# Optimization experiments

Hardware: AMD Instinct MI355X
Metric: run time of the kernel (lower is better)

Reference implementation:

```python
import jax, jax.numpy as jnp
from jax import lax
import numpy as np

EPS = 1e-5  # BatchNorm eps


def setup_inputs() -> dict:
    key = jax.random.key(0)
    ks = jax.random.split(key, 4)
    T, B, C = 256, 128, 1024
    L, H, NCLS = 6, 1024, 1000
    x = jax.random.normal(ks[0], (T, B, C), dtype=jnp.float32)
    W = jax.random.normal(ks[1], (L, C, H), dtype=jnp.float32) * (1.0 / np.sqrt(C))
    b = jnp.zeros((L, H), dtype=jnp.float32)
    gamma = jnp.ones((L, H), dtype=jnp.float32)
    beta = jnp.zeros((L, H), dtype=jnp.float32)
    u = jax.random.uniform(ks[2], (L, H), dtype=jnp.float32)  # recurrent weights in (0, U_bound~1)
    Wc = jax.random.normal(ks[3], (H, NCLS), dtype=jnp.float32) * (1.0 / np.sqrt(H))
    bc = jnp.zeros((NCLS,), dtype=jnp.float32)
    return {"x": x, "W": W, "b": b, "gamma": gamma, "beta": beta, "u": u, "Wc": Wc, "bc": bc}


def _layer(h, Wl, bl, gl, betal, ul):
    # per-timestep dense projection: [T,B,Cin] @ [Cin,H]
    z = jnp.einsum('tbi,ih->tbh', h, Wl) + bl
    # BN over (time, batch) per channel (bn_before, training-mode batch stats)
    mean = jnp.mean(z, axis=(0, 1))
    var = jnp.var(z, axis=(0, 1))
    z = (z - mean) * (gl / jnp.sqrt(var + EPS)) + betal
    # IndRNN diagonal recurrence: h_t = relu(z_t + u * h_{t-1}), h_0 = 0
    T, B, H = z.shape
    def step(hprev, zt):
        hnew = jax.nn.relu(zt + ul * hprev)
        return hnew, hnew
    _, hs = lax.scan(step, jnp.zeros((B, H), dtype=z.dtype), z)
    return hs


def reference(x, W, b, gamma, beta, u, Wc, bc):
    h = x
    for l in range(W.shape[0]):
        h = _layer(h, W[l], b[l], gamma[l], beta[l], u[l])
    # classifier on last timestep
    return h[-1] @ Wc + bc
```

## Files before the change

kernel.cpp:

```cpp
#include <hip/hip_runtime.h>
#include <hip/hip_bf16.h>

#define T_DIM 256
#define B_DIM 128
#define C_DIM 1024
#define H_DIM 1024
#define L_DIM 6
#define NC_DIM 1000
#define M_DIM (T_DIM * B_DIM)
#define BH_DIM (B_DIM * H_DIM)

typedef __attribute__((ext_vector_type(8))) short bf16x8;
typedef __attribute__((ext_vector_type(4))) float f32x4;

__device__ __forceinline__ float bf2f(unsigned short u) {
  union { unsigned int i; float f; } v; v.i = ((unsigned int)u) << 16; return v.f;
}
__device__ __forceinline__ unsigned short f2bf(float f) {
  union { float f; unsigned int i; } v; v.f = f;
  unsigned int r = v.i + 0x7fffu + ((v.i >> 16) & 1u);
  return (unsigned short)(r >> 16);
}

__device__ __forceinline__ void gload_lds16(const void* g, void* l) {
  __builtin_amdgcn_global_load_lds(
      (const __attribute__((address_space(1))) unsigned int*)g,
      (__attribute__((address_space(3))) unsigned int*)l, 16, 0, 0);
}

__global__ __launch_bounds__(256) void f32_to_bf16_kernel(
    const float* __restrict__ in, unsigned short* __restrict__ out, int n4) {
  int stride = gridDim.x * blockDim.x;
  for (int i = blockIdx.x * blockDim.x + threadIdx.x; i < n4; i += stride) {
    float4 v = ((const float4*)in)[i];
    ushort4 o;
    o.x = f2bf(v.x); o.y = f2bf(v.y); o.z = f2bf(v.z); o.w = f2bf(v.w);
    ((ushort4*)out)[i] = o;
  }
}

__global__ __launch_bounds__(256) void wtrans_kernel(
    const float* __restrict__ W, unsigned short* __restrict__ Wt) {
  __shared__ float tile[32][33];
  int l = blockIdx.z;
  const float* Wl = W + (size_t)l * C_DIM * H_DIM;
  unsigned short* Wtl = Wt + (size_t)l * C_DIM * H_DIM;
  int h0 = blockIdx.x * 32, c0 = blockIdx.y * 32;
  int tx = threadIdx.x, ty = threadIdx.y;
#pragma unroll
  for (int i = 0; i < 32; i += 8)
    tile[ty + i][tx] = Wl[(size_t)(c0 + ty + i) * H_DIM + h0 + tx];
  __syncthreads();
#pragma unroll
  for (int i = 0; i < 32; i += 8)
    Wtl[(size_t)(h0 + ty + i) * C_DIM + c0 + tx] = f2bf(tile[tx][ty + i]);
}

#define NT 32

__global__ __launch_bounds__(512, 2) void gemm_kernel(
    const unsigned short* __restrict__ A, const unsigned short* __restrict__ Bt,
    unsigned short* __restrict__ Z, float* __restrict__ psum, float* __restrict__ psqs) {
  extern __shared__ char lds[];
  int bid = blockIdx.x;
  int swz = (bid & 7) * 64 + (bid >> 3);
  int tm = swz >> 2, tn = swz & 3;
  int tid = threadIdx.x;
  int wv = tid >> 6, ln = tid & 63;
  int wm = wv >> 2, wn = wv & 3;

  const char* Asrc = (const char*)A + (size_t)tm * 256 * 2048;
  const char* Bsrc = (const char*)Bt + (size_t)tn * 256 * 2048;
  int p0 = wv * 1024 + ln * 16;
  int p1 = 8192 + wv * 1024 + ln * 16;
  int l0 = p0 ^ (((p0 >> 7) & 3) << 4);
  int l1 = p1 ^ (((p1 >> 7) & 3) << 4);
  int ro0 = (p0 >> 6) * 2048 + (l0 & 63);
  int ro1 = (p1 >> 6) * 2048 + (l1 & 63);
  int dst0 = wv * 1024;
  int dst1 = 8192 + wv * 1024;

  int laneoff = (ln & 15) * 64 + ((((ln >> 4) ^ ((ln & 15) >> 1)) & 3) << 4);

  f32x4 acc[8][4];
  f32x4 zero = {0.f, 0.f, 0.f, 0.f};
#pragma unroll
  for (int m = 0; m < 8; ++m)
#pragma unroll
    for (int n = 0; n < 4; ++n) acc[m][n] = zero;

  auto stage = [&](int t) {
    char* ldsb = lds + ((t & 3) * 32768);
    int ko = t * 64;
    gload_lds16(Asrc + ro0 + ko, ldsb + dst0);
    gload_lds16(Asrc + ro1 + ko, ldsb + dst1);
    gload_lds16(Bsrc + ro0 + ko, ldsb + 16384 + dst0);
    gload_lds16(Bsrc + ro1 + ko, ldsb + 16384 + dst1);
  };

  auto body = [&](int t, bool dostage) {
    const char* buf = lds + ((t & 3) * 32768);
    const char* Ab = buf + wm * 8192;
    const char* Bb = buf + 16384 + wn * 4096;
    bf16x8 bf[4], a0[4], a1[4];
#pragma unroll
    for (int n = 0; n < 4; ++n) bf[n] = *(const bf16x8*)(Bb + n * 1024 + laneoff);
#pragma unroll
    for (int m = 0; m < 4; ++m) a0[m] = *(const bf16x8*)(Ab + m * 1024 + laneoff);
#pragma unroll
    for (int m = 0; m < 4; ++m) a1[m] = *(const bf16x8*)(Ab + 4096 + m * 1024 + laneoff);
    if (dostage) stage(t + 3);
    __builtin_amdgcn_s_setprio(1);
#pragma unroll
    for (int m = 0; m < 4; ++m)
#pragma unroll
      for (int n = 0; n < 4; ++n)
        acc[m][n] = __builtin_amdgcn_mfma_f32_16x16x32_bf16(a0[m], bf[n], acc[m][n], 0, 0, 0);
#pragma unroll
    for (int m = 0; m < 4; ++m)
#pragma unroll
      for (int n = 0; n < 4; ++n)
        acc[m + 4][n] = __builtin_amdgcn_mfma_f32_16x16x32_bf16(a1[m], bf[n], acc[m + 4][n], 0, 0, 0);
    __builtin_amdgcn_s_setprio(0);
  };

  stage(0); stage(1); stage(2);
  asm volatile("s_waitcnt vmcnt(8)" ::: "memory");
  __builtin_amdgcn_s_barrier();

  for (int t = 0; t < NT - 3; ++t) {
    body(t, true);
    asm volatile("s_waitcnt vmcnt(8)" ::: "memory");
    __builtin_amdgcn_s_barrier();
  }
  body(NT - 3, false);
  asm volatile("s_waitcnt vmcnt(4)" ::: "memory");
  __builtin_amdgcn_s_barrier();
  body(NT - 2, false);
  asm volatile("s_waitcnt vmcnt(0)" ::: "memory");
  __builtin_amdgcn_s_barrier();
  body(NT - 1, false);

  float s[4], q[4];
#pragma unroll
  for (int n = 0; n < 4; ++n) {
    float sv = 0.f, qv = 0.f;
#pragma unroll
    for (int m = 0; m < 8; ++m)
#pragma unroll
      for (int r = 0; r < 4; ++r) {
        float v = acc[m][n][r];
        sv += v; qv += v * v;
      }
    s[n] = sv; q[n] = qv;
  }
#pragma unroll
  for (int n = 0; n < 4; ++n) {
    s[n] += __shfl_xor(s[n], 16); s[n] += __shfl_xor(s[n], 32);
    q[n] += __shfl_xor(q[n], 16); q[n] += __shfl_xor(q[n], 32);
  }
  float* red = (float*)lds;
  if (ln < 16) {
#pragma unroll
    for (int n = 0; n < 4; ++n) {
      red[wm * 256 + wn * 64 + n * 16 + ln] = s[n];
      red[512 + wm * 256 + wn * 64 + n * 16 + ln] = q[n];
    }
  }
  __syncthreads();
  if (tid < 256) {
    psum[(size_t)tm * H_DIM + tn * 256 + tid] = red[tid] + red[256 + tid];
  } else {
    int c = tid - 256;
    psqs[(size_t)tm * H_DIM + tn * 256 + c] = red[512 + c] + red[768 + c];
  }
  int r0 = tm * 256 + wm * 128 + ((ln >> 4) << 2);
  int c0 = tn * 256 + wn * 64 + (ln & 15);
#pragma unroll
  for (int m = 0; m < 8; ++m)
#pragma unroll
    for (int n = 0; n < 4; ++n) {
      unsigned short* zp = Z + (size_t)(r0 + m * 16) * H_DIM + c0 + n * 16;
#pragma unroll
      for (int r = 0; r < 4; ++r) zp[(size_t)r * H_DIM] = f2bf(acc[m][n][r]);
    }
}

__global__ __launch_bounds__(256) void bn_finalize_kernel(
    const float* __restrict__ psum, const float* __restrict__ psqs,
    const float* __restrict__ gamma, const float* __restrict__ beta,
    float* __restrict__ ss) {
  int c = blockIdx.x * blockDim.x + threadIdx.x;
  float s = 0.f, q = 0.f;
  for (int i = 0; i < 128; ++i) {
    s += psum[(size_t)i * H_DIM + c];
    q += psqs[(size_t)i * H_DIM + c];
  }
  const float invN = 1.0f / (float)M_DIM;
  float mean = s * invN;
  float var = q * invN - mean * mean;
  float sc = gamma[c] * rsqrtf(var + 1e-5f);
  ss[c] = sc;
  ss[H_DIM + c] = beta[c] - mean * sc;
}

__global__ __launch_bounds__(256) void bn_recur_kernel(
    const unsigned short* __restrict__ Z, const float* __restrict__ ss,
    const float* __restrict__ u, unsigned short* __restrict__ Hout) {
  int i2 = blockIdx.x * 256 + threadIdx.x;
  int h0 = (i2 & (H_DIM / 2 - 1)) * 2;
  float sc0 = ss[h0], sc1 = ss[h0 + 1];
  float sh0 = ss[H_DIM + h0], sh1 = ss[H_DIM + h0 + 1];
  float u0 = u[h0], u1 = u[h0 + 1];
  float hv0 = 0.f, hv1 = 0.f;
  const unsigned int* Zp = (const unsigned int*)Z;
#pragma unroll 8
  for (int t = 0; t < T_DIM; ++t) {
    unsigned int zz = Zp[(size_t)t * (BH_DIM / 2) + i2];
    float z0 = fmaf(bf2f((unsigned short)(zz & 0xffffu)), sc0, sh0);
    float z1 = fmaf(bf2f((unsigned short)(zz >> 16)), sc1, sh1);
    hv0 = fmaxf(fmaf(u0, hv0, z0), 0.f);
    hv1 = fmaxf(fmaf(u1, hv1, z1), 0.f);
    ushort2 o; o.x = f2bf(hv0); o.y = f2bf(hv1);
    ((ushort2*)Hout)[(size_t)t * (BH_DIM / 2) + i2] = o;
  }
}

__global__ __launch_bounds__(256) void classifier_kernel(
    const unsigned short* __restrict__ hlast, const float* __restrict__ Wc,
    const float* __restrict__ bc, float* __restrict__ out) {
  __shared__ float hs[H_DIM];
  int b = blockIdx.y;
  int n = blockIdx.x * 256 + threadIdx.x;
  for (int k = threadIdx.x; k < H_DIM; k += 256)
    hs[k] = bf2f(hlast[(size_t)b * H_DIM + k]);
  __syncthreads();
  if (n < NC_DIM) {
    float acc = bc[n];
#pragma unroll 8
    for (int k = 0; k < H_DIM; ++k)
      acc = fmaf(hs[k], Wc[(size_t)k * NC_DIM + n], acc);
    out[(size_t)b * NC_DIM + n] = acc;
  }
}

extern "C" void kernel_launch(void* const* d_in, const int* in_sizes, int n_in,
                              void* d_out, int out_size, void* d_ws, size_t ws_size,
                              hipStream_t stream) {
  const float* x     = (const float*)d_in[0];
  const float* W     = (const float*)d_in[1];
  const float* gamma = (const float*)d_in[3];
  const float* beta  = (const float*)d_in[4];
  const float* u     = (const float*)d_in[5];
  const float* Wc    = (const float*)d_in[6];
  const float* bc    = (const float*)d_in[7];
  float* out = (float*)d_out;

  const size_t CH = (size_t)C_DIM * H_DIM;
  const size_t MH = (size_t)M_DIM * H_DIM;
  char* p = (char*)d_ws;
  unsigned short* Wt = (unsigned short*)p; p += L_DIM * CH * sizeof(unsigned short);
  unsigned short* Ha = (unsigned short*)p; p += MH * sizeof(unsigned short);
  unsigned short* Hb = (unsigned short*)p; p += MH * sizeof(unsigned short);
  unsigned short* Z  = (unsigned short*)p; p += MH * sizeof(unsigned short);
  float* psum = (float*)p; p += 128 * H_DIM * sizeof(float);
  float* psqs = (float*)p; p += 128 * H_DIM * sizeof(float);
  float* ss   = (float*)p; p += 2 * H_DIM * sizeof(float);

  f32_to_bf16_kernel<<<2048, 256, 0, stream>>>(x, Ha, (int)(MH / 4));
  wtrans_kernel<<<dim3(H_DIM / 32, C_DIM / 32, L_DIM), dim3(32, 8), 0, stream>>>(W, Wt);

  unsigned short* cur = Ha;
  unsigned short* nxt = Hb;
  for (int l = 0; l < L_DIM; ++l) {
    gemm_kernel<<<(M_DIM / 256) * (H_DIM / 256), 512, 131072, stream>>>(
        cur, Wt + (size_t)l * CH, Z, psum, psqs);
    bn_finalize_kernel<<<4, 256, 0, stream>>>(psum, psqs, gamma + (size_t)l * H_DIM,
                                              beta + (size_t)l * H_DIM, ss);
    bn_recur_kernel<<<BH_DIM / 512, 256, 0, stream>>>(Z, ss, u + (size_t)l * H_DIM, nxt);
    unsigned short* tmp = cur; cur = nxt; nxt = tmp;
  }
  classifier_kernel<<<dim3(4, B_DIM), 256, 0, stream>>>(
      cur + (size_t)(T_DIM - 1) * BH_DIM, Wc, bc, out);
}
```

Measured before the change: 782.0 us.

## Shrink GEMM tile to 256x128 with double-buffered LDS for higher occupancy

The GEMM tile shrinks from 256x256 to 256x128, with 8 waves arranged 4x2 and 16 accumulators each instead of 32. The LDS pipeline drops from 4-stage to 2-stage (48KB instead of 128KB), which allows more blocks per CU and doubles the grid. The BN partial-sum reduction is reworked to match the new wave layout, and the recurrence loop unroll goes from 8 to 16. The trade-off is less data reuse per block, more global traffic for the A operand, and a shallower prefetch, since each step now does a full vmcnt(0) wait.

```diff
diff --git a/kernel.cpp b/kernel.cpp
--- a/kernel.cpp
+++ b/kernel.cpp
@@ -58,87 +58,77 @@
 
 #define NT 32
 
-__global__ __launch_bounds__(512, 2) void gemm_kernel(
+__global__ __launch_bounds__(512, 4) void gemm_kernel(
     const unsigned short* __restrict__ A, const unsigned short* __restrict__ Bt,
     unsigned short* __restrict__ Z, float* __restrict__ psum, float* __restrict__ psqs) {
   extern __shared__ char lds[];
   int bid = blockIdx.x;
-  int swz = (bid & 7) * 64 + (bid >> 3);
-  int tm = swz >> 2, tn = swz & 3;
+  int swz = (bid & 7) * 128 + (bid >> 3);
+  int tm = swz >> 3, tn = swz & 7;
   int tid = threadIdx.x;
   int wv = tid >> 6, ln = tid & 63;
-  int wm = wv >> 2, wn = wv & 3;
+  int wm = wv >> 1, wn = wv & 1;
 
   const char* Asrc = (const char*)A + (size_t)tm * 256 * 2048;
-  const char* Bsrc = (const char*)Bt + (size_t)tn * 256 * 2048;
+  const char* Bsrc = (const char*)Bt + (size_t)tn * 128 * 2048;
   int p0 = wv * 1024 + ln * 16;
   int p1 = 8192 + wv * 1024 + ln * 16;
+  int pB = wv * 1024 + ln * 16;
   int l0 = p0 ^ (((p0 >> 7) & 3) << 4);
   int l1 = p1 ^ (((p1 >> 7) & 3) << 4);
+  int lB = pB ^ (((pB >> 7) & 3) << 4);
   int ro0 = (p0 >> 6) * 2048 + (l0 & 63);
   int ro1 = (p1 >> 6) * 2048 + (l1 & 63);
+  int roB = (pB >> 6) * 2048 + (lB & 63);
   int dst0 = wv * 1024;
   int dst1 = 8192 + wv * 1024;
+  int dstB = 16384 + wv * 1024;
 
   int laneoff = (ln & 15) * 64 + ((((ln >> 4) ^ ((ln & 15) >> 1)) & 3) << 4);
 
-  f32x4 acc[8][4];
+  f32x4 acc[4][4];
   f32x4 zero = {0.f, 0.f, 0.f, 0.f};
 #pragma unroll
-  for (int m = 0; m < 8; ++m)
+  for (int m = 0; m < 4; ++m)
 #pragma unroll
     for (int n = 0; n < 4; ++n) acc[m][n] = zero;
 
   auto stage = [&](int t) {
-    char* ldsb = lds + ((t & 3) * 32768);
+    char* ldsb = lds + ((t & 1) * 24576);
     int ko = t * 64;
     gload_lds16(Asrc + ro0 + ko, ldsb + dst0);
     gload_lds16(Asrc + ro1 + ko, ldsb + dst1);
-    gload_lds16(Bsrc + ro0 + ko, ldsb + 16384 + dst0);
-    gload_lds16(Bsrc + ro1 + ko, ldsb + 16384 + dst1);
+    gload_lds16(Bsrc + roB + ko, ldsb + dstB);
   };
 
   auto body = [&](int t, bool dostage) {
-    const char* buf = lds + ((t & 3) * 32768);
-    const char* Ab = buf + wm * 8192;
+    const char* buf = lds + ((t & 1) * 24576);
+    if (dostage) stage(t + 1);
+    const char* Ab = buf + wm * 4096;
     const char* Bb = buf + 16384 + wn * 4096;
-    bf16x8 bf[4], a0[4], a1[4];
-#pragma unroll
-    for (int n = 0; n < 4; ++n) bf[n] = *(const bf16x8*)(Bb + n * 1024 + laneoff);
-#pragma unroll
-    for (int m = 0; m < 4; ++m) a0[m] = *(const bf16x8*)(Ab + m * 1024 + laneoff);
-#pragma unroll
-    for (int m = 0; m < 4; ++m) a1[m] = *(const bf16x8*)(Ab + 4096 + m * 1024 + laneoff);
-    if (dostage) stage(t + 3);
+    bf16x8 a[4], b[4];
+#pragma unroll
+    for (int m = 0; m < 4; ++m) a[m] = *(const bf16x8*)(Ab + m * 1024 + laneoff);
+#pragma unroll
+    for (int n = 0; n < 4; ++n) b[n] = *(const bf16x8*)(Bb + n * 1024 + laneoff);
     __builtin_amdgcn_s_setprio(1);
 #pragma unroll
     for (int m = 0; m < 4; ++m)
 #pragma unroll
       for (int n = 0; n < 4; ++n)
-        acc[m][n] = __builtin_amdgcn_mfma_f32_16x16x32_bf16(a0[m], bf[n], acc[m][n], 0, 0, 0);
-#pragma unroll
-    for (int m = 0; m < 4; ++m)
-#pragma unroll
-      for (int n = 0; n < 4; ++n)
-        acc[m + 4][n] = __builtin_amdgcn_mfma_f32_16x16x32_bf16(a1[m], bf[n], acc[m + 4][n], 0, 0, 0);
+        acc[m][n] = __builtin_amdgcn_mfma_f32_16x16x32_bf16(a[m], b[n], acc[m][n], 0, 0, 0);
     __builtin_amdgcn_s_setprio(0);
   };
 
-  stage(0); stage(1); stage(2);
-  asm volatile("s_waitcnt vmcnt(8)" ::: "memory");
-  __builtin_amdgcn_s_barrier();
-
-  for (int t = 0; t < NT - 3; ++t) {
-    body(t, true);
-    asm volatile("s_waitcnt vmcnt(8)" ::: "memory");
-    __builtin_amdgcn_s_barrier();
-  }
-  body(NT - 3, false);
-  asm volatile("s_waitcnt vmcnt(4)" ::: "memory");
-  __builtin_amdgcn_s_barrier();
-  body(NT - 2, false);
+  stage(0);
   asm volatile("s_waitcnt vmcnt(0)" ::: "memory");
   __builtin_amdgcn_s_barrier();
+
+  for (int t = 0; t < NT - 1; ++t) {
+    body(t, true);
+    asm volatile("s_waitcnt vmcnt(0)" ::: "memory");
+    __builtin_amdgcn_s_barrier();
+  }
   body(NT - 1, false);
 
   float s[4], q[4];
@@ -146,7 +136,7 @@
   for (int n = 0; n < 4; ++n) {
     float sv = 0.f, qv = 0.f;
 #pragma unroll
-    for (int m = 0; m < 8; ++m)
+    for (int m = 0; m < 4; ++m)
 #pragma unroll
       for (int r = 0; r < 4; ++r) {
         float v = acc[m][n][r];
@@ -160,24 +150,27 @@
     q[n] += __shfl_xor(q[n], 16); q[n] += __shfl_xor(q[n], 32);
   }
   float* red = (float*)lds;
+  __syncthreads();
   if (ln < 16) {
 #pragma unroll
     for (int n = 0; n < 4; ++n) {
-      red[wm * 256 + wn * 64 + n * 16 + ln] = s[n];
-      red[512 + wm * 256 + wn * 64 + n * 16 + ln] = q[n];
+      red[wm * 128 + wn * 64 + n * 16 + ln] = s[n];
+      red[512 + wm * 128 + wn * 64 + n * 16 + ln] = q[n];
     }
   }
   __syncthreads();
-  if (tid < 256) {
-    psum[(size_t)tm * H_DIM + tn * 256 + tid] = red[tid] + red[256 + tid];
-  } else {
-    int c = tid - 256;
-    psqs[(size_t)tm * H_DIM + tn * 256 + c] = red[512 + c] + red[768 + c];
-  }
-  int r0 = tm * 256 + wm * 128 + ((ln >> 4) << 2);
-  int c0 = tn * 256 + wn * 64 + (ln & 15);
-#pragma unroll
-  for (int m = 0; m < 8; ++m)
+  if (tid < 128) {
+    psum[(size_t)tm * H_DIM + tn * 128 + tid] =
+        red[tid] + red[128 + tid] + red[256 + tid] + red[384 + tid];
+  } else if (tid < 256) {
+    int c = tid - 128;
+    psqs[(size_t)tm * H_DIM + tn * 128 + c] =
+        red[512 + c] + red[640 + c] + red[768 + c] + red[896 + c];
+  }
+  int r0 = tm * 256 + wm * 64 + ((ln >> 4) << 2);
+  int c0 = tn * 128 + wn * 64 + (ln & 15);
+#pragma unroll
+  for (int m = 0; m < 4; ++m)
 #pragma unroll
     for (int n = 0; n < 4; ++n) {
       unsigned short* zp = Z + (size_t)(r0 + m * 16) * H_DIM + c0 + n * 16;
@@ -214,7 +207,7 @@
   float u0 = u[h0], u1 = u[h0 + 1];
   float hv0 = 0.f, hv1 = 0.f;
   const unsigned int* Zp = (const unsigned int*)Z;
-#pragma unroll 8
+#pragma unroll 16
   for (int t = 0; t < T_DIM; ++t) {
     unsigned int zz = Zp[(size_t)t * (BH_DIM / 2) + i2];
     float z0 = fmaf(bf2f((unsigned short)(zz & 0xffffu)), sc0, sh0);
@@ -273,7 +266,7 @@
   unsigned short* cur = Ha;
   unsigned short* nxt = Hb;
   for (int l = 0; l < L_DIM; ++l) {
-    gemm_kernel<<<(M_DIM / 256) * (H_DIM / 256), 512, 131072, stream>>>(
+    gemm_kernel<<<(M_DIM / 256) * (H_DIM / 128), 512, 49152, stream>>>(
         cur, Wt + (size_t)l * CH, Z, psum, psqs);
     bn_finalize_kernel<<<4, 256, 0, stream>>>(psum, psqs, gamma + (size_t)l * H_DIM,
                                               beta + (size_t)l * H_DIM, ss);
```

Measured after the change: 784.9 us. Within noise of the previous version (+0.4%).

## Split GEMM stage loads around MFMA halves and prefetch recurrence inputs in batches

Applied to the files above, without the earlier changes.

The GEMM main loop now issues the A-tile global-to-LDS loads before the first half of the MFMAs and the B-tile loads before the second half. Each half is bracketed by extra workgroup barriers, so memory traffic is interleaved with compute rather than issued all at once. The BN+recurrence kernel now double-buffers 32 timesteps of Z in registers, so many loads are in flight while the serial scan runs. This adds barriers and register pressure in exchange for better latency hiding.

```diff
diff --git a/kernel.cpp b/kernel.cpp
--- a/kernel.cpp
+++ b/kernel.cpp
@@ -89,11 +89,15 @@
 #pragma unroll
     for (int n = 0; n < 4; ++n) acc[m][n] = zero;
 
-  auto stage = [&](int t) {
+  auto stageA = [&](int t) {
     char* ldsb = lds + ((t & 3) * 32768);
     int ko = t * 64;
     gload_lds16(Asrc + ro0 + ko, ldsb + dst0);
     gload_lds16(Asrc + ro1 + ko, ldsb + dst1);
+  };
+  auto stageB = [&](int t) {
+    char* ldsb = lds + ((t & 3) * 32768);
+    int ko = t * 64;
     gload_lds16(Bsrc + ro0 + ko, ldsb + 16384 + dst0);
     gload_lds16(Bsrc + ro1 + ko, ldsb + 16384 + dst1);
   };
@@ -107,15 +111,20 @@
     for (int n = 0; n < 4; ++n) bf[n] = *(const bf16x8*)(Bb + n * 1024 + laneoff);
 #pragma unroll
     for (int m = 0; m < 4; ++m) a0[m] = *(const bf16x8*)(Ab + m * 1024 + laneoff);
-#pragma unroll
-    for (int m = 0; m < 4; ++m) a1[m] = *(const bf16x8*)(Ab + 4096 + m * 1024 + laneoff);
-    if (dostage) stage(t + 3);
+    if (dostage) stageA(t + 3);
+    __builtin_amdgcn_s_barrier();
     __builtin_amdgcn_s_setprio(1);
 #pragma unroll
     for (int m = 0; m < 4; ++m)
 #pragma unroll
       for (int n = 0; n < 4; ++n)
         acc[m][n] = __builtin_amdgcn_mfma_f32_16x16x32_bf16(a0[m], bf[n], acc[m][n], 0, 0, 0);
+    __builtin_amdgcn_s_setprio(0);
+    __builtin_amdgcn_s_barrier();
+#pragma unroll
+    for (int m = 0; m < 4; ++m) a1[m] = *(const bf16x8*)(Ab + 4096 + m * 1024 + laneoff);
+    if (dostage) stageB(t + 3);
+    __builtin_amdgcn_s_setprio(1);
 #pragma unroll
     for (int m = 0; m < 4; ++m)
 #pragma unroll
@@ -124,7 +133,7 @@
     __builtin_amdgcn_s_setprio(0);
   };
 
-  stage(0); stage(1); stage(2);
+  stageA(0); stageB(0); stageA(1); stageB(1); stageA(2); stageB(2);
   asm volatile("s_waitcnt vmcnt(8)" ::: "memory");
   __builtin_amdgcn_s_barrier();
 
@@ -213,16 +222,41 @@
   float sh0 = ss[H_DIM + h0], sh1 = ss[H_DIM + h0 + 1];
   float u0 = u[h0], u1 = u[h0 + 1];
   float hv0 = 0.f, hv1 = 0.f;
-  const unsigned int* Zp = (const unsigned int*)Z;
-#pragma unroll 8
-  for (int t = 0; t < T_DIM; ++t) {
-    unsigned int zz = Zp[(size_t)t * (BH_DIM / 2) + i2];
-    float z0 = fmaf(bf2f((unsigned short)(zz & 0xffffu)), sc0, sh0);
-    float z1 = fmaf(bf2f((unsigned short)(zz >> 16)), sc1, sh1);
-    hv0 = fmaxf(fmaf(u0, hv0, z0), 0.f);
-    hv1 = fmaxf(fmaf(u1, hv1, z1), 0.f);
-    ushort2 o; o.x = f2bf(hv0); o.y = f2bf(hv1);
-    ((ushort2*)Hout)[(size_t)t * (BH_DIM / 2) + i2] = o;
+  const size_t ST = BH_DIM / 2;
+  const unsigned int* Zt = (const unsigned int*)Z + i2;
+  unsigned int* Ht = (unsigned int*)Hout + i2;
+
+  unsigned int za[32], zb[32];
+#pragma unroll
+  for (int j = 0; j < 32; ++j) za[j] = Zt[(size_t)j * ST];
+
+#pragma unroll
+  for (int blk = 0; blk < 4; ++blk) {
+    int tA = blk * 64;
+#pragma unroll
+    for (int j = 0; j < 32; ++j) zb[j] = Zt[(size_t)(tA + 32 + j) * ST];
+#pragma unroll
+    for (int j = 0; j < 32; ++j) {
+      unsigned int zz = za[j];
+      float z0 = fmaf(bf2f((unsigned short)(zz & 0xffffu)), sc0, sh0);
+      float z1 = fmaf(bf2f((unsigned short)(zz >> 16)), sc1, sh1);
+      hv0 = fmaxf(fmaf(u0, hv0, z0), 0.f);
+      hv1 = fmaxf(fmaf(u1, hv1, z1), 0.f);
+      Ht[(size_t)(tA + j) * ST] = ((unsigned int)f2bf(hv1) << 16) | f2bf(hv0);
+    }
+    if (blk < 3) {
+#pragma unroll
+      for (int j = 0; j < 32; ++j) za[j] = Zt[(size_t)(tA + 64 + j) * ST];
+    }
+#pragma unroll
+    for (int j = 0; j < 32; ++j) {
+      unsigned int zz = zb[j];
+      float z0 = fmaf(bf2f((unsigned short)(zz & 0xffffu)), sc0, sh0);
+      float z1 = fmaf(bf2f((unsigned short)(zz >> 16)), sc1, sh1);
+      hv0 = fmaxf(fmaf(u0, hv0, z0), 0.f);
+      hv1 = fmaxf(fmaf(u1, hv1, z1), 0.f);
+      Ht[(size_t)(tA + 32 + j) * ST] = ((unsigned int)f2bf(hv1) << 16) | f2bf(hv0);
+    }
   }
 }
 
```

Result: faster. 760.0 us (-2.8%).
